# Kernel optimization log

Hardware: AMD Instinct MI355X
Metric: run time of the kernel (lower is better)

The kernel has to match this reference:

```python
import jax, jax.numpy as jnp
import numpy as np

B, D, K = 32, 20000, 16
HH, EH, L, DH = 128, 256, 32, 128


def setup_inputs() -> dict:
    key = jax.random.key(0)
    ks = jax.random.split(key, 16)
    g = lambda k, shape, fan_in: jax.random.normal(k, shape, jnp.float32) / np.sqrt(fan_in)
    return {
        "x": jax.random.normal(ks[0], (B, D), jnp.float32),
        "mask": jax.random.randint(ks[1], (B, D), 0, 2, jnp.int32),
        # encoder feature embedding/bias (shared with decoder)
        "F_embed": jax.random.normal(ks[2], (D, K), jnp.float32),
        "f_bias": jnp.zeros((D, 1), jnp.float32),
        # h_layer: Linear(1+K+1 -> HH), Linear(HH -> K)
        "W1": g(ks[3], (2 + K, HH), 2 + K), "b1": jnp.zeros((HH,), jnp.float32),
        "W2": g(ks[4], (HH, K), HH), "b2": jnp.zeros((K,), jnp.float32),
        # encoder_mlp: Linear(K -> EH), Linear(EH -> 2L)
        "We1": g(ks[5], (K, EH), K), "be1": jnp.zeros((EH,), jnp.float32),
        "We2": g(ks[6], (EH, 2 * L), EH), "be2": jnp.zeros((2 * L,), jnp.float32),
        # z_processor: Linear(L -> DH)
        "Wz": g(ks[7], (L, DH), L), "bz": jnp.zeros((DH,), jnp.float32),
        # j_layer: Linear(DH+K+1 -> DH), Linear(DH -> 1)
        "Wj1": g(ks[8], (DH + K + 1, DH), DH + K + 1), "bj1": jnp.zeros((DH,), jnp.float32),
        "Wj2": g(ks[9], (DH, 1), DH), "bj2": jnp.zeros((1,), jnp.float32),
    }


def reference(x, mask, F_embed, f_bias, W1, b1, W2, b2, We1, be1, We2, be2,
              Wz, bz, Wj1, bj1, Wj2, bj2):
    relu = jax.nn.relu
    bsz = x.shape[0]
    # ---- encoder: per-feature shared h_layer ----
    # h_input = [x_j, F_j, b_j] : (B, D, 2+K)
    h_in = jnp.concatenate([
        x[:, :, None],
        jnp.broadcast_to(F_embed[None], (bsz, D, K)),
        jnp.broadcast_to(f_bias[None], (bsz, D, 1)),
    ], axis=-1)
    h = relu(h_in @ W1 + b1)          # (B, D, HH)
    h = relu(h @ W2 + b2)             # (B, D, K)
    c = jnp.sum(h * mask.astype(jnp.float32)[:, :, None], axis=1)  # (B, K)
    enc = relu(c @ We1 + be1) @ We2 + be2                          # (B, 2L)
    mu, logvar = enc[:, :L], enc[:, L:]
    # eval mode: z = mu
    z = mu
    # ---- decoder: broadcast-concat shared j_layer ----
    pz = relu(z @ Wz + bz)            # (B, DH)
    j_in = jnp.concatenate([
        jnp.broadcast_to(pz[:, None, :], (bsz, D, DH)),
        jnp.broadcast_to(F_embed[None], (bsz, D, K)),
        jnp.broadcast_to(f_bias[None], (bsz, D, 1)),
    ], axis=-1)                       # (B, D, DH+K+1)
    rec = (relu(j_in @ Wj1 + bj1) @ Wj2 + bj2)[..., 0]  # (B, D)
    return rec, mu, logvar
```

## Files before the change

### kernel.cpp

```cpp
#include <hip/hip_runtime.h>
#include <hip/hip_bf16.h>

#define Dn 20000
#define Bn 32

typedef short bf8_t __attribute__((ext_vector_type(8)));
typedef float f32x4 __attribute__((ext_vector_type(4)));

static __device__ __forceinline__ short f2bf(float f) {
    __hip_bfloat16 h = __float2bfloat16(f);
    return __builtin_bit_cast(short, h);
}


__global__ __launch_bounds__(256) void kB(const float* __restrict__ x,
                                          const int* __restrict__ mask,
                                          const float* __restrict__ F_embed,
                                          const float* __restrict__ f_bias,
                                          const float* __restrict__ W1,
                                          const float* __restrict__ b1,
                                          const float* __restrict__ W2,
                                          const float* __restrict__ b2,
                                          float* __restrict__ partial)
{
    const int t = threadIdx.x;
    const int w = t >> 6;
    const int l = t & 63;
    const int bhalf = w & 1;
    const int dsub  = w >> 1;
    const int d0 = blockIdx.x * 16;

    __shared__ float f1s[16][128];
    __shared__ float fes[16][17];
    __shared__ float xs[528];
    __shared__ float ms[528];
    __shared__ float red[512];

    {
        const int dl = t >> 4, i = t & 15;
        fes[dl][i] = F_embed[(size_t)(d0 + dl) * 16 + i];
        if (t < 16) fes[t][16] = f_bias[d0 + t];
    }
#pragma unroll
    for (int i = 0; i < 2; ++i) {
        const int idx = t + i * 256;
        const int dl = idx & 15, b = idx >> 4;
        xs[dl * 33 + b] = x[b * Dn + d0 + dl];
        ms[dl * 33 + b] = (float)mask[b * Dn + d0 + dl];
    }

    const int ko = (l >> 4) * 8;
    float w1f[4][8];
#pragma unroll
    for (int s = 0; s < 4; ++s)
#pragma unroll
        for (int e = 0; e < 8; ++e) w1f[s][e] = W1[s * 32 + ko + e];
    bf8_t bfr[4];
#pragma unroll
    for (int s = 0; s < 4; ++s)
#pragma unroll
        for (int e = 0; e < 8; ++e) bfr[s][e] = f2bf(W2[(s * 32 + ko + e) * 16 + (l & 15)]);
    const float b2v = b2[l & 15];

    __syncthreads();

#pragma unroll
    for (int e = 0; e < 8; ++e) {
        const int idx = t + e * 256;
        const int dl = idx >> 7, k = idx & 127;
        float acc = fmaf(fes[dl][16], W1[17 * 128 + k], b1[k]);
#pragma unroll
        for (int i = 0; i < 16; ++i) acc = fmaf(fes[dl][i], W1[(1 + i) * 128 + k], acc);
        f1s[dl][k] = acc;
    }
    __syncthreads();

    f32x4 cacc = {0.f, 0.f, 0.f, 0.f};
    for (int i = 0; i < 8; ++i) {
        const int dl = dsub * 8 + i;
        const float xv = xs[dl * 33 + bhalf * 16 + (l & 15)];
        f32x4 acc = {0.f, 0.f, 0.f, 0.f};
#pragma unroll
        for (int s = 0; s < 4; ++s) {
            const float4 fa = *(const float4*)(&f1s[dl][s * 32 + ko]);
            const float4 fb = *(const float4*)(&f1s[dl][s * 32 + ko + 4]);
            bf8_t af;
            af[0] = f2bf(fmaxf(fmaf(xv, w1f[s][0], fa.x), 0.f));
            af[1] = f2bf(fmaxf(fmaf(xv, w1f[s][1], fa.y), 0.f));
            af[2] = f2bf(fmaxf(fmaf(xv, w1f[s][2], fa.z), 0.f));
            af[3] = f2bf(fmaxf(fmaf(xv, w1f[s][3], fa.w), 0.f));
            af[4] = f2bf(fmaxf(fmaf(xv, w1f[s][4], fb.x), 0.f));
            af[5] = f2bf(fmaxf(fmaf(xv, w1f[s][5], fb.y), 0.f));
            af[6] = f2bf(fmaxf(fmaf(xv, w1f[s][6], fb.z), 0.f));
            af[7] = f2bf(fmaxf(fmaf(xv, w1f[s][7], fb.w), 0.f));
            acc = __builtin_amdgcn_mfma_f32_16x16x32_bf16(af, bfr[s], acc, 0, 0, 0);
        }
#pragma unroll
        for (int r = 0; r < 4; ++r) {
            const float mvr = ms[dl * 33 + bhalf * 16 + (l >> 4) * 4 + r];
            cacc[r] = fmaf(mvr, fmaxf(acc[r] + b2v, 0.f), cacc[r]);
        }
    }

    const int base = bhalf * 256 + (l >> 4) * 64 + (l & 15);
    if (dsub == 0) {
        red[base]      = cacc[0];
        red[base + 16] = cacc[1];
        red[base + 32] = cacc[2];
        red[base + 48] = cacc[3];
    }
    __syncthreads();
    if (dsub == 1) {
        red[base]      += cacc[0];
        red[base + 16] += cacc[1];
        red[base + 32] += cacc[2];
        red[base + 48] += cacc[3];
    }
    __syncthreads();
    float* __restrict__ po = partial + blockIdx.x * 512;
    po[t]       = red[t];
    po[t + 256] = red[t + 256];
}

__global__ __launch_bounds__(256) void kC(const float* __restrict__ partial,
                                          const float* __restrict__ We1,
                                          const float* __restrict__ be1,
                                          const float* __restrict__ We2,
                                          const float* __restrict__ be2,
                                          const float* __restrict__ Wz,
                                          const float* __restrict__ bz,
                                          const float* __restrict__ Wj1,
                                          const float* __restrict__ bj1,
                                          float* __restrict__ out,
                                          float* __restrict__ basews)
{
    const int b = blockIdx.x;
    const int t = threadIdx.x;
    __shared__ float rsum[16][17];
    __shared__ float cb[16];
    __shared__ float henc[256];
    __shared__ float ep[4][64];
    __shared__ float zl[32];
    __shared__ float pzl[128];
    __shared__ float jp[2][128];

    {
        const int j = t & 15, g = t >> 4;
        float s = 0.f;
        for (int r = g; r < 1250; r += 16) s += partial[r * 512 + b * 16 + j];
        rsum[g][j] = s;
    }
    __syncthreads();
    if (t < 16) {
        float a = 0.f;
#pragma unroll
        for (int g = 0; g < 16; ++g) a += rsum[g][t];
        cb[t] = a;
    }
    __syncthreads();

    {
        float a = be1[t];
#pragma unroll
        for (int i = 0; i < 16; ++i) a = fmaf(cb[i], We1[i * 256 + t], a);
        henc[t] = fmaxf(a, 0.f);
    }
    __syncthreads();

    {
        const int o = t & 63, s = t >> 6;
        float a = 0.f;
#pragma unroll 8
        for (int i = 0; i < 64; ++i) a = fmaf(henc[s * 64 + i], We2[(s * 64 + i) * 64 + o], a);
        ep[s][o] = a;
    }
    __syncthreads();
    if (t < 64) {
        const float e = be2[t] + ep[0][t] + ep[1][t] + ep[2][t] + ep[3][t];
        if (t < 32) { out[640000 + b * 32 + t] = e; zl[t] = e; }
        else        { out[641024 + b * 32 + (t - 32)] = e; }
    }
    __syncthreads();

    if (t < 128) {
        float a = bz[t];
#pragma unroll 8
        for (int i = 0; i < 32; ++i) a = fmaf(zl[i], Wz[i * 128 + t], a);
        pzl[t] = fmaxf(a, 0.f);
    }
    __syncthreads();

    {
        const int k = t & 127, s = t >> 7;
        float a = 0.f;
#pragma unroll 8
        for (int i = 0; i < 64; ++i) a = fmaf(pzl[s * 64 + i], Wj1[(s * 64 + i) * 128 + k], a);
        jp[s][k] = a;
    }
    __syncthreads();
    if (t < 128) basews[b * 128 + t] = bj1[t] + jp[0][t] + jp[1][t];
}

__global__ __launch_bounds__(256) void kA2(const float* __restrict__ F_embed,
                                           const float* __restrict__ f_bias,
                                           const float* __restrict__ Wj1,
                                           float* __restrict__ FjT)
{
    const int d  = blockIdx.x * 256 + threadIdx.x;
    const int kg = blockIdx.y * 8;
    if (d >= Dn) return;
    const float4* fe4 = (const float4*)(F_embed + d * 16);
    float fe[16];
    {
        float4 a = fe4[0], b = fe4[1], c = fe4[2], e = fe4[3];
        fe[0]=a.x; fe[1]=a.y; fe[2]=a.z; fe[3]=a.w;
        fe[4]=b.x; fe[5]=b.y; fe[6]=b.z; fe[7]=b.w;
        fe[8]=c.x; fe[9]=c.y; fe[10]=c.z; fe[11]=c.w;
        fe[12]=e.x; fe[13]=e.y; fe[14]=e.z; fe[15]=e.w;
    }
    const float fb = f_bias[d];
#pragma unroll
    for (int j = 0; j < 8; ++j) {
        const int k = kg + j;
        float acc = fb * Wj1[144 * 128 + k];
#pragma unroll
        for (int i = 0; i < 16; ++i) acc = fmaf(fe[i], Wj1[(128 + i) * 128 + k], acc);
        FjT[k * Dn + d] = acc;
    }
}

__global__ __launch_bounds__(256) void kD(const float* __restrict__ FjT,
                                          const float* __restrict__ basews,
                                          const float* __restrict__ Wj2,
                                          const float* __restrict__ bj2,
                                          float* __restrict__ rec)
{
    const int d  = blockIdx.x * 256 + threadIdx.x;
    const int bq = blockIdx.y * 4;
    if (d >= Dn) return;
    const float* __restrict__ bA = basews + (bq + 0) * 128;
    const float* __restrict__ bB = basews + (bq + 1) * 128;
    const float* __restrict__ bC = basews + (bq + 2) * 128;
    const float* __restrict__ bD = basews + (bq + 3) * 128;
    float a0 = 0.f, a1 = 0.f, a2 = 0.f, a3 = 0.f;
#pragma unroll 8
    for (int k = 0; k < 128; ++k) {
        const float fj = FjT[k * Dn + d];
        const float w  = Wj2[k];
        a0 = fmaf(fmaxf(fj + bA[k], 0.f), w, a0);
        a1 = fmaf(fmaxf(fj + bB[k], 0.f), w, a1);
        a2 = fmaf(fmaxf(fj + bC[k], 0.f), w, a2);
        a3 = fmaf(fmaxf(fj + bD[k], 0.f), w, a3);
    }
    const float bj = bj2[0];
    rec[(bq + 0) * Dn + d] = a0 + bj;
    rec[(bq + 1) * Dn + d] = a1 + bj;
    rec[(bq + 2) * Dn + d] = a2 + bj;
    rec[(bq + 3) * Dn + d] = a3 + bj;
}

extern "C" void kernel_launch(void* const* d_in, const int* in_sizes, int n_in,
                              void* d_out, int out_size, void* d_ws, size_t ws_size,
                              hipStream_t stream)
{
    const float* x       = (const float*)d_in[0];
    const int*   mask    = (const int*)d_in[1];
    const float* F_embed = (const float*)d_in[2];
    const float* f_bias  = (const float*)d_in[3];
    const float* W1      = (const float*)d_in[4];
    const float* b1      = (const float*)d_in[5];
    const float* W2      = (const float*)d_in[6];
    const float* b2      = (const float*)d_in[7];
    const float* We1     = (const float*)d_in[8];
    const float* be1     = (const float*)d_in[9];
    const float* We2     = (const float*)d_in[10];
    const float* be2     = (const float*)d_in[11];
    const float* Wz      = (const float*)d_in[12];
    const float* bz      = (const float*)d_in[13];
    const float* Wj1     = (const float*)d_in[14];
    const float* bj1     = (const float*)d_in[15];
    const float* Wj2     = (const float*)d_in[16];
    const float* bj2     = (const float*)d_in[17];
    float* out = (float*)d_out;
    float* ws  = (float*)d_ws;

    float* FjT     = ws;
    float* partial = ws + 2560000;
    float* basews  = ws + 3200000;

    kB <<<1250, 256, 0, stream>>>(x, mask, F_embed, f_bias, W1, b1, W2, b2, partial);
    kC <<<32,   256, 0, stream>>>(partial, We1, be1, We2, be2, Wz, bz, Wj1, bj1, out, basews);
    kA2<<<dim3(79, 16), 256, 0, stream>>>(F_embed, f_bias, Wj1, FjT);
    kD <<<dim3(79, 8),  256, 0, stream>>>(FjT, basews, Wj2, bj2, out);
}
```

Measured before the change: 159.6 us.

## Fuse F-projection and decoder output kernels, recompute Fj in registers

Merges the kernel that projected F_embed through Wj1 into a transposed FjT buffer with the decoder kernel that consumed it. Each thread now computes its feature's 128 Fj values in chunks of 16 in registers and applies them to 8 batch rows, with the basews rows and Wj2 staged in shared memory. This removes the 10 MB FjT write and its re-read, plus one kernel launch. In exchange, Fj is recomputed once for each of the 4 batch groups, and the grid shrinks to 316 blocks, which may leave the GPU under-occupied.

```diff
diff --git a/kernel.cpp b/kernel.cpp
--- a/kernel.cpp
+++ b/kernel.cpp
@@ -201,62 +201,73 @@
     if (t < 128) basews[b * 128 + t] = bj1[t] + jp[0][t] + jp[1][t];
 }
 
-__global__ __launch_bounds__(256) void kA2(const float* __restrict__ F_embed,
+__global__ __launch_bounds__(256) void kDF(const float* __restrict__ F_embed,
                                            const float* __restrict__ f_bias,
                                            const float* __restrict__ Wj1,
-                                           float* __restrict__ FjT)
+                                           const float* __restrict__ basews,
+                                           const float* __restrict__ Wj2,
+                                           const float* __restrict__ bj2,
+                                           float* __restrict__ rec)
 {
-    const int d  = blockIdx.x * 256 + threadIdx.x;
-    const int kg = blockIdx.y * 8;
-    if (d >= Dn) return;
-    const float4* fe4 = (const float4*)(F_embed + d * 16);
+    const int t  = threadIdx.x;
+    const int d  = blockIdx.x * 256 + t;
+    const int b0 = blockIdx.y * 8;
+
+    __shared__ float bls[8][128];
+    __shared__ float wj2s[128];
+
+#pragma unroll
+    for (int i = 0; i < 4; ++i) {
+        const int e = t + i * 256;
+        bls[e >> 7][e & 127] = basews[(b0 + (e >> 7)) * 128 + (e & 127)];
+    }
+    if (t < 128) wj2s[t] = Wj2[t];
+    __syncthreads();
+
+    const int dc = d < Dn ? d : (Dn - 1);
     float fe[16];
     {
+        const float4* fe4 = (const float4*)(F_embed + (size_t)dc * 16);
         float4 a = fe4[0], b = fe4[1], c = fe4[2], e = fe4[3];
         fe[0]=a.x; fe[1]=a.y; fe[2]=a.z; fe[3]=a.w;
         fe[4]=b.x; fe[5]=b.y; fe[6]=b.z; fe[7]=b.w;
         fe[8]=c.x; fe[9]=c.y; fe[10]=c.z; fe[11]=c.w;
         fe[12]=e.x; fe[13]=e.y; fe[14]=e.z; fe[15]=e.w;
     }
-    const float fb = f_bias[d];
-#pragma unroll
-    for (int j = 0; j < 8; ++j) {
-        const int k = kg + j;
-        float acc = fb * Wj1[144 * 128 + k];
-#pragma unroll
-        for (int i = 0; i < 16; ++i) acc = fmaf(fe[i], Wj1[(128 + i) * 128 + k], acc);
-        FjT[k * Dn + d] = acc;
-    }
-}
-
-__global__ __launch_bounds__(256) void kD(const float* __restrict__ FjT,
-                                          const float* __restrict__ basews,
-                                          const float* __restrict__ Wj2,
-                                          const float* __restrict__ bj2,
-                                          float* __restrict__ rec)
-{
-    const int d  = blockIdx.x * 256 + threadIdx.x;
-    const int bq = blockIdx.y * 4;
-    if (d >= Dn) return;
-    const float* __restrict__ bA = basews + (bq + 0) * 128;
-    const float* __restrict__ bB = basews + (bq + 1) * 128;
-    const float* __restrict__ bC = basews + (bq + 2) * 128;
-    const float* __restrict__ bD = basews + (bq + 3) * 128;
-    float a0 = 0.f, a1 = 0.f, a2 = 0.f, a3 = 0.f;
-#pragma unroll 8
-    for (int k = 0; k < 128; ++k) {
-        const float fj = FjT[k * Dn + d];
-        const float w  = Wj2[k];
-        a0 = fmaf(fmaxf(fj + bA[k], 0.f), w, a0);
-        a1 = fmaf(fmaxf(fj + bB[k], 0.f), w, a1);
-        a2 = fmaf(fmaxf(fj + bC[k], 0.f), w, a2);
-        a3 = fmaf(fmaxf(fj + bD[k], 0.f), w, a3);
-    }
-    const float bj = bj2[0];
-    rec[(bq + 0) * Dn + d] = a0 + bj;
-    rec[(bq + 1) * Dn + d] = a1 + bj;
-    rec[(bq + 2) * Dn + d] = a2 + bj;
-    rec[(bq + 3) * Dn + d] = a3 + bj;
+    const float fb = f_bias[dc];
+
+    float acc[8];
+#pragma unroll
+    for (int bi = 0; bi < 8; ++bi) acc[bi] = 0.f;
+
+    for (int kt = 0; kt < 8; ++kt) {
+        float fj[16];
+#pragma unroll
+        for (int j = 0; j < 16; ++j) {
+            const int k = kt * 16 + j;
+            float a = fb * Wj1[144 * 128 + k];
+#pragma unroll
+            for (int i = 0; i < 16; ++i) a = fmaf(fe[i], Wj1[(128 + i) * 128 + k], a);
+            fj[j] = a;
+        }
+#pragma unroll
+        for (int bi = 0; bi < 8; ++bi) {
+            float s = acc[bi];
+#pragma unroll
+            for (int j = 0; j < 16; ++j) {
+                const int k = kt * 16 + j;
+                s = fmaf(fmaxf(fj[j] + bls[bi][k], 0.f), wj2s[k], s);
+            }
+            acc[bi] = s;
+        }
+    }
+
+    if (d < Dn) {
+        const float bj = bj2[0];
+#pragma unroll
+        for (int bi = 0; bi < 8; ++bi)
+            rec[(size_t)(b0 + bi) * Dn + d] = acc[bi] + bj;
+    }
 }
 
 extern "C" void kernel_launch(void* const* d_in, const int* in_sizes, int n_in,
@@ -284,12 +295,10 @@
     float* out = (float*)d_out;
     float* ws  = (float*)d_ws;
 
-    float* FjT     = ws;
-    float* partial = ws + 2560000;
-    float* basews  = ws + 3200000;
+    float* partial = ws;
+    float* basews  = ws + 640000;
 
     kB <<<1250, 256, 0, stream>>>(x, mask, F_embed, f_bias, W1, b1, W2, b2, partial);
     kC <<<32,   256, 0, stream>>>(partial, We1, be1, We2, be2, Wz, bz, Wj1, bj1, out, basews);
-    kA2<<<dim3(79, 16), 256, 0, stream>>>(F_embed, f_bias, Wj1, FjT);
-    kD <<<dim3(79, 8),  256, 0, stream>>>(FjT, basews, Wj2, bj2, out);
-}
+    kDF<<<dim3(79, 4), 256, 0, stream>>>(F_embed, f_bias, Wj1, basews, Wj2, bj2, out);
+}
```

Result: slower. 163.3 us (+2.4%).
